# Performance work log

Measured on AMD Instinct MI355X. Metric: run time of the kernel, lower is better.

The kernel has to match this reference:

```python
import jax, jax.numpy as jnp
import numpy as np

T = 256   # time steps
F = 64    # features per step
H = 32    # LSTM hidden size
FORGET_BIAS = 1.0  # TF LSTMCell default


def setup_inputs() -> dict:
    key = jax.random.key(0)
    k1, k2, k3 = jax.random.split(key, 3)
    B = 16384
    x = jax.random.normal(k1, (B, T * F), dtype=jnp.float32)
    W_lstm = jax.random.normal(k2, (F + H, 4 * H), dtype=jnp.float32) * 0.1
    b_lstm = jnp.zeros((4 * H,), dtype=jnp.float32)
    W_dense = jax.random.normal(k3, (H, 1), dtype=jnp.float32) * 0.1
    b_dense = jnp.zeros((1,), dtype=jnp.float32)
    return {"x": x, "W_lstm": W_lstm, "b_lstm": b_lstm,
            "W_dense": W_dense, "b_dense": b_dense}


def reference(x, W_lstm, b_lstm, W_dense, b_dense):
    B = x.shape[0]
    # [B, T*F] -> [T, B, F] for scan over time
    xs = x.reshape(B, T, F).transpose(1, 0, 2)

    def step(carry, x_t):
        c, h = carry
        # TF LSTMCell: concat([inputs, h]) @ kernel + bias, gate order i, j, f, o
        gates = jnp.concatenate([x_t, h], axis=-1) @ W_lstm + b_lstm
        i, j, f, o = jnp.split(gates, 4, axis=-1)
        c_new = c * jax.nn.sigmoid(f + FORGET_BIAS) + jax.nn.sigmoid(i) * jnp.tanh(j)
        h_new = jnp.tanh(c_new) * jax.nn.sigmoid(o)
        return (c_new, h_new), None

    c0 = jnp.zeros((B, H), dtype=x.dtype)
    h0 = jnp.zeros((B, H), dtype=x.dtype)
    (c_T, h_T), _ = jax.lax.scan(step, (c0, h0), xs)

    # dense(1) + ELU on the final hidden state, then flatten like predict()
    out = jax.nn.elu(h_T @ W_dense + b_dense)
    return out.reshape(-1)
```

## Files before the change

### kernel.cpp

```cpp
#include <hip/hip_runtime.h>

#define T_STEPS 256
#define F_IN 64

typedef __bf16 bf16x8 __attribute__((ext_vector_type(8)));
typedef float f32x4 __attribute__((ext_vector_type(4)));

__device__ __forceinline__ float sigmoid_f(float x) {
    return __builtin_amdgcn_rcpf(1.0f + __builtin_amdgcn_exp2f(-1.44269504f * x));
}
__device__ __forceinline__ float tanh_f(float x) {
    return 1.0f - 2.0f * __builtin_amdgcn_rcpf(1.0f + __builtin_amdgcn_exp2f(2.88539008f * x));
}

__global__ __launch_bounds__(256, 1)
void lstm_fused(const float* __restrict__ x,
                const float* __restrict__ Wl,
                const float* __restrict__ bl,
                const float* __restrict__ Wd,
                const float* __restrict__ bd,
                float* __restrict__ out)
{
    __shared__ __align__(16) __bf16 h_all[4][16][32];
    const int lane = threadIdx.x & 63;
    const int wid  = threadIdx.x >> 6;
    const int cl   = lane & 15;
    const int g4   = lane >> 4;
    const int rowBase = blockIdx.x * 64 + wid * 16;

    __bf16 (*h_buf)[32] = h_all[wid];

    bf16x8 wfrag[3][8];
#pragma unroll
    for (int kc = 0; kc < 3; ++kc) {
#pragma unroll
        for (int cf = 0; cf < 8; ++cf) {
            bf16x8 v;
#pragma unroll
            for (int j = 0; j < 8; ++j)
                v[j] = (__bf16)Wl[(kc * 32 + g4 * 8 + j) * 128 + cf * 16 + cl];
            wfrag[kc][cf] = v;
        }
    }

    float bias[8];
#pragma unroll
    for (int cf = 0; cf < 8; ++cf) bias[cf] = bl[cf * 16 + cl];

    const float wd0 = Wd[cl], wd1 = Wd[cl + 16];
    const float bdv = bd[0];

    *reinterpret_cast<f32x4*>(reinterpret_cast<char*>(&h_buf[0][0]) + lane * 16) =
        f32x4{0.f, 0.f, 0.f, 0.f};
    asm volatile("s_waitcnt lgkmcnt(0)" ::: "memory");

    float c_st[2][4] = {{0.f,0.f,0.f,0.f},{0.f,0.f,0.f,0.f}};
    float h_last[2][4];

    const float* xrow = x + (size_t)(rowBase + cl) * (size_t)(T_STEPS * F_IN);

    f32x4 xa[4], xb[4];

#define LOAD_X(BUF, TT) do {                                                  \
        const float* _p = xrow + (TT) * F_IN + g4 * 8;                        \
        BUF[0] = *reinterpret_cast<const f32x4*>(_p);                         \
        BUF[1] = *reinterpret_cast<const f32x4*>(_p + 4);                     \
        BUF[2] = *reinterpret_cast<const f32x4*>(_p + 32);                    \
        BUF[3] = *reinterpret_cast<const f32x4*>(_p + 36);                    \
    } while (0)

#define STEP(TT, XCUR) do {                                                   \
                                       \
        bf16x8 ax0, ax1;                                                      \
        _Pragma("unroll")                                                     \
        for (int j = 0; j < 4; ++j) {                                         \
            ax0[j]     = (__bf16)XCUR[0][j];                                  \
            ax0[4 + j] = (__bf16)XCUR[1][j];                                  \
            ax1[j]     = (__bf16)XCUR[2][j];                                  \
            ax1[4 + j] = (__bf16)XCUR[3][j];                                  \
        }                                                                     \
                                 \
        if ((TT) + 2 < T_STEPS) { LOAD_X(XCUR, (TT) + 2); }                   \
                        \
        bf16x8 ah = *reinterpret_cast<bf16x8*>(&h_buf[cl][g4 * 8]);           \
        f32x4 acc[8];                                                         \
        _Pragma("unroll")                                                     \
        for (int cf = 0; cf < 8; ++cf) {                                      \
            f32x4 a = {bias[cf], bias[cf], bias[cf], bias[cf]};               \
            a = __builtin_amdgcn_mfma_f32_16x16x32_bf16(ax0, wfrag[0][cf], a, 0, 0, 0); \
            a = __builtin_amdgcn_mfma_f32_16x16x32_bf16(ax1, wfrag[1][cf], a, 0, 0, 0); \
            a = __builtin_amdgcn_mfma_f32_16x16x32_bf16(ah,  wfrag[2][cf], a, 0, 0, 0); \
            acc[cf] = a;                                                      \
        }                                                                     \
        \
        _Pragma("unroll")                                                     \
        for (int half = 0; half < 2; ++half) {                                \
            _Pragma("unroll")                                                 \
            for (int r = 0; r < 4; ++r) {                                     \
                float gi = acc[0 + half][r];                                  \
                float gj = acc[2 + half][r];                                  \
                float gf = acc[4 + half][r];                                  \
                float go = acc[6 + half][r];                                  \
                float sf = sigmoid_f(gf + 1.0f);                              \
                float si = sigmoid_f(gi);                                     \
                float tj = tanh_f(gj);                                        \
                float cn = c_st[half][r] * sf + si * tj;                      \
                float tc = tanh_f(cn);                                        \
                float so = sigmoid_f(go);                                     \
                float hh = tc * so;                                           \
                c_st[half][r] = cn;                                           \
                h_last[half][r] = hh;                                         \
                h_buf[g4 * 4 + r][half * 16 + cl] = (__bf16)hh;               \
            }                                                                 \
        }                                                                     \
        asm volatile("s_waitcnt lgkmcnt(0)" ::: "memory");                    \
    } while (0)

    LOAD_X(xa, 0);
    LOAD_X(xb, 1);

    for (int t = 0; t < T_STEPS; t += 2) {
        STEP(t, xa);
        STEP(t + 1, xb);
    }

    float s[4];
#pragma unroll
    for (int r = 0; r < 4; ++r) {
        float v = h_last[0][r] * wd0 + h_last[1][r] * wd1;
#pragma unroll
        for (int m = 1; m < 16; m <<= 1) v += __shfl_xor(v, m, 64);
        s[r] = v;
    }
    if (cl == 0) {
#pragma unroll
        for (int r = 0; r < 4; ++r) {
            float z = s[r] + bdv;
            out[rowBase + g4 * 4 + r] = z > 0.f ? z : (__expf(z) - 1.0f);
        }
    }
#undef STEP
#undef LOAD_X
}

extern "C" void kernel_launch(void* const* d_in, const int* in_sizes, int n_in,
                              void* d_out, int out_size, void* d_ws, size_t ws_size,
                              hipStream_t stream) {
    const float* x  = (const float*)d_in[0];
    const float* Wl = (const float*)d_in[1];
    const float* bl = (const float*)d_in[2];
    const float* Wd = (const float*)d_in[3];
    const float* bd = (const float*)d_in[4];
    float* out = (float*)d_out;

    const int rows = out_size;
    const int grid = (rows + 63) / 64;
    hipLaunchKernelGGL(lstm_fused, dim3(grid), dim3(256), 0, stream,
                       x, Wl, bl, Wd, bd, out);
}
```

Measured before the change: 258.6 us.

## Stream x via async global-to-LDS ring and pass hidden state through shuffles

Replaces the per-step register prefetch of x with a 4-slot LDS ring filled by global_load_lds with a 3-step lookahead and a swizzled layout. The MFMA operands are transposed so each lane's outputs map to batch rows, which lets h be repacked into the next step's A operand with lane shuffles instead of an LDS round trip and wait. Bias and the log2e scaling are folded into precomputed FMA constants, and the final dense reduction shrinks to two xor-shuffles. This aims to take LDS synchronisation and load latency off the serial recurrence, at the cost of more complex indexing and reliance on vmcnt counting.

```diff
diff --git a/kernel.cpp b/kernel.cpp
--- a/kernel.cpp
+++ b/kernel.cpp
@@ -1,16 +1,24 @@
 #include <hip/hip_runtime.h>
+#include <stdint.h>
 
 #define T_STEPS 256
 #define F_IN 64
+#define L2E 1.44269504f
 
 typedef __bf16 bf16x8 __attribute__((ext_vector_type(8)));
 typedef float f32x4 __attribute__((ext_vector_type(4)));
-
-__device__ __forceinline__ float sigmoid_f(float x) {
-    return __builtin_amdgcn_rcpf(1.0f + __builtin_amdgcn_exp2f(-1.44269504f * x));
-}
-__device__ __forceinline__ float tanh_f(float x) {
-    return 1.0f - 2.0f * __builtin_amdgcn_rcpf(1.0f + __builtin_amdgcn_exp2f(2.88539008f * x));
+typedef uint32_t u32;
+typedef uint32_t u32x4 __attribute__((ext_vector_type(4)));
+
+#define GLDS16(gp, lp)                                                         \
+    __builtin_amdgcn_global_load_lds(                                          \
+        (const __attribute__((address_space(1))) unsigned int*)(gp),           \
+        (__attribute__((address_space(3))) unsigned int*)(lp), 16, 0, 0)
+
+__device__ __forceinline__ u32 pk2(float lo, float hi) {
+    unsigned short a = __builtin_bit_cast(unsigned short, (__bf16)lo);
+    unsigned short b = __builtin_bit_cast(unsigned short, (__bf16)hi);
+    return (u32)a | ((u32)b << 16);
 }
 
 __global__ __launch_bounds__(256, 1)
@@ -21,126 +29,159 @@
                 const float* __restrict__ bd,
                 float* __restrict__ out)
 {
-    __shared__ __align__(16) __bf16 h_all[4][16][32];
+    __shared__ __align__(16) float xlds[4][4][1024];
     const int lane = threadIdx.x & 63;
     const int wid  = threadIdx.x >> 6;
     const int cl   = lane & 15;
     const int g4   = lane >> 4;
     const int rowBase = blockIdx.x * 64 + wid * 16;
 
-    __bf16 (*h_buf)[32] = h_all[wid];
-
     bf16x8 wfrag[3][8];
 #pragma unroll
     for (int kc = 0; kc < 3; ++kc) {
 #pragma unroll
-        for (int cf = 0; cf < 8; ++cf) {
+        for (int gt = 0; gt < 8; ++gt) {
             bf16x8 v;
 #pragma unroll
             for (int j = 0; j < 8; ++j)
-                v[j] = (__bf16)Wl[(kc * 32 + g4 * 8 + j) * 128 + cf * 16 + cl];
-            wfrag[kc][cf] = v;
+                v[j] = (__bf16)Wl[(kc * 32 + g4 * 8 + j) * 128 + gt * 16 + cl];
+            wfrag[kc][gt] = v;
         }
     }
 
-    float bias[8];
-#pragma unroll
-    for (int cf = 0; cf < 8; ++cf) bias[cf] = bl[cf * 16 + cl];
-
-    const float wd0 = Wd[cl], wd1 = Wd[cl + 16];
-    const float bdv = bd[0];
-
-    *reinterpret_cast<f32x4*>(reinterpret_cast<char*>(&h_buf[0][0]) + lane * 16) =
-        f32x4{0.f, 0.f, 0.f, 0.f};
-    asm volatile("s_waitcnt lgkmcnt(0)" ::: "memory");
-
+    float KI[2][4], KJ[2][4], KF[2][4], KO[2][4];
+#pragma unroll
+    for (int uh = 0; uh < 2; ++uh) {
+        f32x4 bi = *(const f32x4*)(bl +   0 + uh * 16 + g4 * 4);
+        f32x4 bj = *(const f32x4*)(bl +  32 + uh * 16 + g4 * 4);
+        f32x4 bf = *(const f32x4*)(bl +  64 + uh * 16 + g4 * 4);
+        f32x4 bo = *(const f32x4*)(bl +  96 + uh * 16 + g4 * 4);
+#pragma unroll
+        for (int r = 0; r < 4; ++r) {
+            KI[uh][r] = -L2E * bi[r];
+            KJ[uh][r] =  2.0f * L2E * bj[r];
+            KF[uh][r] = -L2E * (bf[r] + 1.0f);
+            KO[uh][r] = -L2E * bo[r];
+        }
+    }
+    const f32x4 wdv0 = *(const f32x4*)(Wd + g4 * 4);
+    const f32x4 wdv1 = *(const f32x4*)(Wd + 16 + g4 * 4);
+    const float bd0 = bd[0];
+
+    const float* gbase = x + (size_t)(rowBase + (lane >> 2)) * (size_t)(T_STEPS * F_IN)
+                           + (size_t)(((lane & 3) ^ ((lane >> 3) & 3)) * 4);
+
+    const int swz = (cl >> 1) & 3;
+    const int c0  = ((g4 & 1) * 2)     ^ swz;
+    const int c1  = ((g4 & 1) * 2 + 1) ^ swz;
+    const int kA  = (g4 >> 1) * 256 + cl * 16;
+    const int kB  = kA + 512;
+
+    asm volatile("s_waitcnt vmcnt(0)" ::: "memory");
+    __builtin_amdgcn_sched_barrier(0);
+
+#pragma unroll
+    for (int s = 0; s < 3; ++s) {
+        const float* gp = gbase + s * F_IN;
+        GLDS16(gp,      &xlds[wid][s][0]);
+        GLDS16(gp + 16, &xlds[wid][s][256]);
+        GLDS16(gp + 32, &xlds[wid][s][512]);
+        GLDS16(gp + 48, &xlds[wid][s][768]);
+    }
+
+    const f32x4 z4 = {0.f, 0.f, 0.f, 0.f};
     float c_st[2][4] = {{0.f,0.f,0.f,0.f},{0.f,0.f,0.f,0.f}};
-    float h_last[2][4];
-
-    const float* xrow = x + (size_t)(rowBase + cl) * (size_t)(T_STEPS * F_IN);
-
-    f32x4 xa[4], xb[4];
-
-#define LOAD_X(BUF, TT) do {                                                  \
-        const float* _p = xrow + (TT) * F_IN + g4 * 8;                        \
-        BUF[0] = *reinterpret_cast<const f32x4*>(_p);                         \
-        BUF[1] = *reinterpret_cast<const f32x4*>(_p + 4);                     \
-        BUF[2] = *reinterpret_cast<const f32x4*>(_p + 32);                    \
-        BUF[3] = *reinterpret_cast<const f32x4*>(_p + 36);                    \
-    } while (0)
-
-#define STEP(TT, XCUR) do {                                                   \
-                                       \
-        bf16x8 ax0, ax1;                                                      \
-        _Pragma("unroll")                                                     \
-        for (int j = 0; j < 4; ++j) {                                         \
-            ax0[j]     = (__bf16)XCUR[0][j];                                  \
-            ax0[4 + j] = (__bf16)XCUR[1][j];                                  \
-            ax1[j]     = (__bf16)XCUR[2][j];                                  \
-            ax1[4 + j] = (__bf16)XCUR[3][j];                                  \
-        }                                                                     \
-                                 \
-        if ((TT) + 2 < T_STEPS) { LOAD_X(XCUR, (TT) + 2); }                   \
-                        \
-        bf16x8 ah = *reinterpret_cast<bf16x8*>(&h_buf[cl][g4 * 8]);           \
-        f32x4 acc[8];                                                         \
-        _Pragma("unroll")                                                     \
-        for (int cf = 0; cf < 8; ++cf) {                                      \
-            f32x4 a = {bias[cf], bias[cf], bias[cf], bias[cf]};               \
-            a = __builtin_amdgcn_mfma_f32_16x16x32_bf16(ax0, wfrag[0][cf], a, 0, 0, 0); \
-            a = __builtin_amdgcn_mfma_f32_16x16x32_bf16(ax1, wfrag[1][cf], a, 0, 0, 0); \
-            a = __builtin_amdgcn_mfma_f32_16x16x32_bf16(ah,  wfrag[2][cf], a, 0, 0, 0); \
-            acc[cf] = a;                                                      \
-        }                                                                     \
-        \
-        _Pragma("unroll")                                                     \
-        for (int half = 0; half < 2; ++half) {                                \
-            _Pragma("unroll")                                                 \
-            for (int r = 0; r < 4; ++r) {                                     \
-                float gi = acc[0 + half][r];                                  \
-                float gj = acc[2 + half][r];                                  \
-                float gf = acc[4 + half][r];                                  \
-                float go = acc[6 + half][r];                                  \
-                float sf = sigmoid_f(gf + 1.0f);                              \
-                float si = sigmoid_f(gi);                                     \
-                float tj = tanh_f(gj);                                        \
-                float cn = c_st[half][r] * sf + si * tj;                      \
-                float tc = tanh_f(cn);                                        \
-                float so = sigmoid_f(go);                                     \
-                float hh = tc * so;                                           \
-                c_st[half][r] = cn;                                           \
-                h_last[half][r] = hh;                                         \
-                h_buf[g4 * 4 + r][half * 16 + cl] = (__bf16)hh;               \
-            }                                                                 \
-        }                                                                     \
-        asm volatile("s_waitcnt lgkmcnt(0)" ::: "memory");                    \
-    } while (0)
-
-    LOAD_X(xa, 0);
-    LOAD_X(xb, 1);
-
-    for (int t = 0; t < T_STEPS; t += 2) {
-        STEP(t, xa);
-        STEP(t + 1, xb);
-    }
-
-    float s[4];
+    float hl[2][4]   = {{0.f,0.f,0.f,0.f},{0.f,0.f,0.f,0.f}};
+    u32x4 ahw = {0u, 0u, 0u, 0u};
+
+    const int srcA = cl + 32 * (g4 & 1);
+    const int srcB = srcA + 16;
+    const int sel  = g4 >> 1;
+
+#define STEP(TT, SLOT) do {                                                    \
+    const int tpf = ((TT) + 3 < T_STEPS) ? (TT) + 3 : T_STEPS - 1;             \
+    const float* gp = gbase + tpf * F_IN;                                      \
+    GLDS16(gp,      &xlds[wid][((SLOT)+3)&3][0]);                              \
+    GLDS16(gp + 16, &xlds[wid][((SLOT)+3)&3][256]);                            \
+    GLDS16(gp + 32, &xlds[wid][((SLOT)+3)&3][512]);                            \
+    GLDS16(gp + 48, &xlds[wid][((SLOT)+3)&3][768]);                            \
+    asm volatile("s_waitcnt vmcnt(12)" ::: "memory");                          \
+    __builtin_amdgcn_sched_barrier(0);                                         \
+    const float* sl = &xlds[wid][SLOT][0];                                     \
+    f32x4 xr0 = *(const f32x4*)(sl + kA + c0 * 4);                             \
+    f32x4 xr1 = *(const f32x4*)(sl + kA + c1 * 4);                             \
+    f32x4 xr2 = *(const f32x4*)(sl + kB + c0 * 4);                             \
+    f32x4 xr3 = *(const f32x4*)(sl + kB + c1 * 4);                             \
+    bf16x8 ax0, ax1;                                                           \
+    _Pragma("unroll")                                                          \
+    for (int j = 0; j < 4; ++j) {                                              \
+        ax0[j]     = (__bf16)xr0[j];                                           \
+        ax0[4 + j] = (__bf16)xr1[j];                                           \
+        ax1[j]     = (__bf16)xr2[j];                                           \
+        ax1[4 + j] = (__bf16)xr3[j];                                           \
+    }                                                                          \
+    bf16x8 ah = __builtin_bit_cast(bf16x8, ahw);                               \
+    f32x4 acc[8];                                                              \
+    _Pragma("unroll")                                                          \
+    for (int gt = 0; gt < 8; ++gt) {                                           \
+        f32x4 a = __builtin_amdgcn_mfma_f32_16x16x32_bf16(wfrag[0][gt], ax0, z4, 0, 0, 0); \
+        a = __builtin_amdgcn_mfma_f32_16x16x32_bf16(wfrag[1][gt], ax1, a, 0, 0, 0);        \
+        a = __builtin_amdgcn_mfma_f32_16x16x32_bf16(wfrag[2][gt], ah,  a, 0, 0, 0);        \
+        acc[gt] = a;                                                           \
+    }                                                                          \
+    _Pragma("unroll")                                                          \
+    for (int uh = 0; uh < 2; ++uh) {                                           \
+        _Pragma("unroll")                                                      \
+        for (int r = 0; r < 4; ++r) {                                          \
+            float gi = acc[uh][r];                                             \
+            float gj = acc[2 + uh][r];                                         \
+            float gf = acc[4 + uh][r];                                         \
+            float go = acc[6 + uh][r];                                         \
+            float sf = __builtin_amdgcn_rcpf(1.0f + __builtin_amdgcn_exp2f(__builtin_fmaf(gf, -L2E, KF[uh][r]))); \
+            float si = __builtin_amdgcn_rcpf(1.0f + __builtin_amdgcn_exp2f(__builtin_fmaf(gi, -L2E, KI[uh][r]))); \
+            float tj = 1.0f - 2.0f * __builtin_amdgcn_rcpf(1.0f + __builtin_amdgcn_exp2f(__builtin_fmaf(gj, 2.0f * L2E, KJ[uh][r]))); \
+            float cn = __builtin_fmaf(c_st[uh][r], sf, si * tj);               \
+            float tc = 1.0f - 2.0f * __builtin_amdgcn_rcpf(1.0f + __builtin_amdgcn_exp2f(2.0f * L2E * cn)); \
+            float so = __builtin_amdgcn_rcpf(1.0f + __builtin_amdgcn_exp2f(__builtin_fmaf(go, -L2E, KO[uh][r]))); \
+            float hh = tc * so;                                                \
+            c_st[uh][r] = cn;                                                  \
+            hl[uh][r] = hh;                                                    \
+        }                                                                      \
+    }                                                                          \
+    u32 P0 = pk2(hl[0][0], hl[0][1]);                                          \
+    u32 P1 = pk2(hl[0][2], hl[0][3]);                                          \
+    u32 P2 = pk2(hl[1][0], hl[1][1]);                                          \
+    u32 P3 = pk2(hl[1][2], hl[1][3]);                                          \
+    int A0 = __shfl((int)P0, srcA, 64), A1 = __shfl((int)P1, srcA, 64);        \
+    int A2 = __shfl((int)P2, srcA, 64), A3 = __shfl((int)P3, srcA, 64);        \
+    int B0 = __shfl((int)P0, srcB, 64), B1 = __shfl((int)P1, srcB, 64);        \
+    int B2 = __shfl((int)P2, srcB, 64), B3 = __shfl((int)P3, srcB, 64);        \
+    ahw[0] = (u32)(sel ? A2 : A0);                                             \
+    ahw[1] = (u32)(sel ? A3 : A1);                                             \
+    ahw[2] = (u32)(sel ? B2 : B0);                                             \
+    ahw[3] = (u32)(sel ? B3 : B1);                                             \
+} while (0)
+
+    for (int t = 0; t < T_STEPS; t += 4) {
+        STEP(t,     0);
+        STEP(t + 1, 1);
+        STEP(t + 2, 2);
+        STEP(t + 3, 3);
+    }
+#undef STEP
+
+    float v = 0.f;
 #pragma unroll
     for (int r = 0; r < 4; ++r) {
-        float v = h_last[0][r] * wd0 + h_last[1][r] * wd1;
-#pragma unroll
-        for (int m = 1; m < 16; m <<= 1) v += __shfl_xor(v, m, 64);
-        s[r] = v;
-    }
-    if (cl == 0) {
-#pragma unroll
-        for (int r = 0; r < 4; ++r) {
-            float z = s[r] + bdv;
-            out[rowBase + g4 * 4 + r] = z > 0.f ? z : (__expf(z) - 1.0f);
-        }
-    }
-#undef STEP
-#undef LOAD_X
+        v = __builtin_fmaf(hl[0][r], wdv0[r], v);
+        v = __builtin_fmaf(hl[1][r], wdv1[r], v);
+    }
+    v += __shfl_xor(v, 16, 64);
+    v += __shfl_xor(v, 32, 64);
+    if (lane < 16) {
+        float z = v + bd0;
+        out[rowBase + lane] = z > 0.f ? z : (__expf(z) - 1.0f);
+    }
 }
 
 extern "C" void kernel_launch(void* const* d_in, const int* in_sizes, int n_in,
```

After: 257.5 us. About the same (-0.4%).
